# Kernel optimization log

Hardware: AMD Instinct MI355X
Metric: run time of the kernel (lower is better)

Reference implementation:

```python
import jax, jax.numpy as jnp
import numpy as np

M, L = 8, 4            # modules x layers -> N = 32 (module,layer) grids
B, H, W = 16, 128, 128  # batch, grid_height, grid_width
E = 256                # number of axonal connections
N = M * L
SPACINGS = (1, 2)      # multi-scale grid spacings ('local', 'global')
EXC_RATIO, EXC_VAL, INH_VAL = 0.8, 1.0, -0.5
CONN_STRENGTH = 0.1


def setup_inputs() -> dict:
    key = jax.random.key(0)
    k_sp, k_mask, k_w, k_src, k_dst = jax.random.split(key, 5)
    spikes = (jax.random.uniform(k_sp, (N, B, H, W)) < 0.1).astype(jnp.float32)
    # excitatory/inhibitory mask per source node (torch.where(rand < ratio, exc, inh))
    exc_mask = jnp.where(jax.random.uniform(k_mask, (N, H, W)) < EXC_RATIO,
                         jnp.float32(EXC_VAL), jnp.float32(INH_VAL))
    # per-connection learned weight grid: randn(H, W) * strength
    conn_weight = jax.random.normal(k_w, (E, H, W), dtype=jnp.float32) * CONN_STRENGTH
    conn_src = jax.random.randint(k_src, (E,), 0, N, dtype=jnp.int32)
    conn_dst = jax.random.randint(k_dst, (E,), 0, N, dtype=jnp.int32)
    scale_weights = jnp.array([1.0, 0.5], dtype=jnp.float32)
    return {"spikes": spikes, "exc_mask": exc_mask, "conn_weight": conn_weight,
            "scale_weights": scale_weights, "conn_src": conn_src, "conn_dst": conn_dst}


def reference(spikes, exc_mask, conn_weight, scale_weights, conn_src, conn_dst):
    # --- AxonalConnections.forward: modulate, weight, scatter-add per connection ---
    modulated = spikes * exc_mask[:, None, :, :]                 # [N,B,H,W]
    msgs = modulated[conn_src] * conn_weight[:, None, :, :]      # [E,B,H,W]
    axonal = jax.ops.segment_sum(msgs, conn_dst, num_segments=N)  # [N,B,H,W]
    # --- MultiScaleGrid.forward: avg layers per module, shift-add by spacing ---
    avg = spikes.reshape(M, L, B, H, W).mean(axis=1)             # [M,B,H,W]
    grid = jnp.zeros_like(avg)
    for si, p in enumerate(SPACINGS):
        w = scale_weights[si]
        grid = grid.at[p:].add(avg[:-p] * w)   # src i = j - p
        grid = grid.at[:-p].add(avg[p:] * w)   # src i = j + p
    # --- _combine_axonal_and_grid: grid signal broadcast to all layers of module ---
    combined = axonal + jnp.repeat(grid, L, axis=0)              # [N,B,H,W]
    return combined
```

## Files before the change

### kernel.cpp

```cpp
#include <hip/hip_runtime.h>
#include <stdint.h>

#define NMOD 8
#define NLAY 4
#define NN   32
#define NB   16
#define HW   16384
#define BHW  262144
#define NE   256
#define NT   256
#define NGRP 4

__device__ __forceinline__ float lo_bf(uint32_t u) {
    union { uint32_t u32; float f; } v; v.u32 = u << 16; return v.f;
}
__device__ __forceinline__ float hi_bf(uint32_t u) {
    union { uint32_t u32; float f; } v; v.u32 = u & 0xffff0000u; return v.f;
}
__device__ __forceinline__ uint32_t pack_trunc(float a, float b) {
    union { float f; uint32_t u; } x, y; x.f = a; y.f = b;
    return (x.u >> 16) | (y.u & 0xffff0000u);
}
__device__ __forceinline__ uint32_t f2bf(float f) {
    union { float ff; uint32_t u; } v; v.ff = f;
    uint32_t u = v.u;
    u += 0x7fffu + ((u >> 16) & 1u);
    return u >> 16;
}

struct ScsSmem {
    uint32_t mod[NN * NT];
    int off[NN + 1];
    int cnt[NN];
    int pair[NE];
};

extern "C" __global__ void __launch_bounds__(NT) scs_axon_grid_kernel(
    const void* __restrict__ d_spikes,
    const void* __restrict__ d_mask,
    const void* __restrict__ d_connw,
    const void* __restrict__ d_scale,
    const int*  __restrict__ conn_src,
    const int*  __restrict__ conn_dst,
    void*       __restrict__ d_outp)
{
    __shared__ ScsSmem sm;

    const int tid   = threadIdx.x;
    const int idx   = blockIdx.x;
    const int chunk = (idx & 7) + 8 * ((idx >> 9) & 3);
    const int mid   = (idx >> 3) & 63;
    const int b     = mid & 15;
    const int ng    = mid >> 4;
    const int n0    = ng * (NN / NGRP);
    const int hw0   = chunk * (2 * NT) + tid * 2;
    const int hwd   = hw0 >> 1;
    const int spw   = (b * HW + hw0) >> 1;

    const bool is_f32 = (*(const uint32_t*)d_scale) == 0x3F800000u;

    const int my_s = conn_src[tid];
    const int my_d = conn_dst[tid];
    if (tid < NN) sm.cnt[tid] = 0;
    __syncthreads();
    atomicAdd(&sm.cnt[my_d], 1);
    __syncthreads();
    if (tid == 0) {
        int a = 0;
        for (int n = 0; n < NN; ++n) { sm.off[n] = a; a += sm.cnt[n]; }
        sm.off[NN] = a;
    }
    __syncthreads();
    if (tid < NN) sm.cnt[tid] = 0;
    __syncthreads();
    {
        int pos = sm.off[my_d] + atomicAdd(&sm.cnt[my_d], 1);
        sm.pair[pos] = (my_s << 8) | tid;
    }

    float avg0[NMOD], avg1[NMOD];
#pragma unroll
    for (int m = 0; m < NMOD; ++m) { avg0[m] = 0.f; avg1[m] = 0.f; }

    float w1, w2;
    if (is_f32) {
        const float* sc = (const float*)d_scale;
        w1 = sc[0]; w2 = sc[1];
        const float2* sp = (const float2*)d_spikes;
        const float2* mk = (const float2*)d_mask;
#pragma unroll
        for (int n = 0; n < NN; ++n) {
            float2 s = sp[n * (BHW / 2) + spw];
            float2 m = mk[n * (HW / 2) + hwd];
            sm.mod[n * NT + tid] = pack_trunc(s.x * m.x, s.y * m.y);
            avg0[n >> 2] += s.x;
            avg1[n >> 2] += s.y;
        }
    } else {
        const uint16_t* sc = (const uint16_t*)d_scale;
        w1 = lo_bf((uint32_t)sc[0]); w2 = lo_bf((uint32_t)sc[1]);
        const uint32_t* sp = (const uint32_t*)d_spikes;
        const uint32_t* mk = (const uint32_t*)d_mask;
#pragma unroll
        for (int n = 0; n < NN; ++n) {
            uint32_t su = sp[n * (BHW / 2) + spw];
            uint32_t mu = mk[n * (HW / 2) + hwd];
            float s0 = lo_bf(su), s1 = hi_bf(su);
            sm.mod[n * NT + tid] = pack_trunc(s0 * lo_bf(mu), s1 * hi_bf(mu));
            avg0[n >> 2] += s0;
            avg1[n >> 2] += s1;
        }
    }

    float g0[NMOD], g1[NMOD];
#pragma unroll
    for (int m = 0; m < NMOD; ++m) {
        float t0 = 0.f, t1 = 0.f, u0 = 0.f, u1 = 0.f;
        if (m >= 1)        { t0 += avg0[m - 1]; t1 += avg1[m - 1]; }
        if (m + 1 < NMOD)  { t0 += avg0[m + 1]; t1 += avg1[m + 1]; }
        if (m >= 2)        { u0 += avg0[m - 2]; u1 += avg1[m - 2]; }
        if (m + 2 < NMOD)  { u0 += avg0[m + 2]; u1 += avg1[m + 2]; }
        g0[m] = (t0 * w1 + u0 * w2) * 0.25f;
        g1[m] = (t1 * w1 + u1 * w2) * 0.25f;
    }

    __syncthreads();

    if (is_f32) {
        const float2* cw  = (const float2*)d_connw;
        float2*       out = (float2*)d_outp;
#pragma unroll
        for (int i = 0; i < NN / NGRP; ++i) {
            const int n = n0 + i;
            float a0 = g0[n >> 2], a1 = g1[n >> 2];
            const int beg = sm.off[n], end = sm.off[n + 1];
            for (int k = beg; k < end; ++k) {
                const int pk = sm.pair[k];
                float2   wv = cw[(pk & 0xff) * (HW / 2) + hwd];
                uint32_t mv = sm.mod[(pk >> 8) * NT + tid];
                a0 = fmaf(lo_bf(mv), wv.x, a0);
                a1 = fmaf(hi_bf(mv), wv.y, a1);
            }
            float2 o; o.x = a0; o.y = a1;
            out[n * (BHW / 2) + spw] = o;
        }
    } else {
        const uint32_t* cw  = (const uint32_t*)d_connw;
        uint32_t*       out = (uint32_t*)d_outp;
#pragma unroll
        for (int i = 0; i < NN / NGRP; ++i) {
            const int n = n0 + i;
            float a0 = g0[n >> 2], a1 = g1[n >> 2];
            const int beg = __builtin_amdgcn_readfirstlane(sm.off[n]);
            const int end = __builtin_amdgcn_readfirstlane(sm.off[n + 1]);
            int k = beg;
            for (; k + 8 <= end; k += 8) {
                const int p0 = __builtin_amdgcn_readfirstlane(sm.pair[k]);
                const int p1 = __builtin_amdgcn_readfirstlane(sm.pair[k + 1]);
                const int p2 = __builtin_amdgcn_readfirstlane(sm.pair[k + 2]);
                const int p3 = __builtin_amdgcn_readfirstlane(sm.pair[k + 3]);
                const int p4 = __builtin_amdgcn_readfirstlane(sm.pair[k + 4]);
                const int p5 = __builtin_amdgcn_readfirstlane(sm.pair[k + 5]);
                const int p6 = __builtin_amdgcn_readfirstlane(sm.pair[k + 6]);
                const int p7 = __builtin_amdgcn_readfirstlane(sm.pair[k + 7]);
                uint32_t wa = cw[(p0 & 0xff) * (HW / 2) + hwd];
                uint32_t wb = cw[(p1 & 0xff) * (HW / 2) + hwd];
                uint32_t wc = cw[(p2 & 0xff) * (HW / 2) + hwd];
                uint32_t wd = cw[(p3 & 0xff) * (HW / 2) + hwd];
                uint32_t we = cw[(p4 & 0xff) * (HW / 2) + hwd];
                uint32_t wf = cw[(p5 & 0xff) * (HW / 2) + hwd];
                uint32_t wg = cw[(p6 & 0xff) * (HW / 2) + hwd];
                uint32_t wh = cw[(p7 & 0xff) * (HW / 2) + hwd];
                uint32_t ma = sm.mod[(p0 >> 8) * NT + tid];
                uint32_t mb = sm.mod[(p1 >> 8) * NT + tid];
                uint32_t mc = sm.mod[(p2 >> 8) * NT + tid];
                uint32_t md = sm.mod[(p3 >> 8) * NT + tid];
                uint32_t me = sm.mod[(p4 >> 8) * NT + tid];
                uint32_t mf = sm.mod[(p5 >> 8) * NT + tid];
                uint32_t mg = sm.mod[(p6 >> 8) * NT + tid];
                uint32_t mh = sm.mod[(p7 >> 8) * NT + tid];
                a0 = fmaf(lo_bf(ma), lo_bf(wa), a0); a1 = fmaf(hi_bf(ma), hi_bf(wa), a1);
                a0 = fmaf(lo_bf(mb), lo_bf(wb), a0); a1 = fmaf(hi_bf(mb), hi_bf(wb), a1);
                a0 = fmaf(lo_bf(mc), lo_bf(wc), a0); a1 = fmaf(hi_bf(mc), hi_bf(wc), a1);
                a0 = fmaf(lo_bf(md), lo_bf(wd), a0); a1 = fmaf(hi_bf(md), hi_bf(wd), a1);
                a0 = fmaf(lo_bf(me), lo_bf(we), a0); a1 = fmaf(hi_bf(me), hi_bf(we), a1);
                a0 = fmaf(lo_bf(mf), lo_bf(wf), a0); a1 = fmaf(hi_bf(mf), hi_bf(wf), a1);
                a0 = fmaf(lo_bf(mg), lo_bf(wg), a0); a1 = fmaf(hi_bf(mg), hi_bf(wg), a1);
                a0 = fmaf(lo_bf(mh), lo_bf(wh), a0); a1 = fmaf(hi_bf(mh), hi_bf(wh), a1);
            }
            for (; k + 4 <= end; k += 4) {
                const int p0 = __builtin_amdgcn_readfirstlane(sm.pair[k]);
                const int p1 = __builtin_amdgcn_readfirstlane(sm.pair[k + 1]);
                const int p2 = __builtin_amdgcn_readfirstlane(sm.pair[k + 2]);
                const int p3 = __builtin_amdgcn_readfirstlane(sm.pair[k + 3]);
                uint32_t wa = cw[(p0 & 0xff) * (HW / 2) + hwd];
                uint32_t wb = cw[(p1 & 0xff) * (HW / 2) + hwd];
                uint32_t wc = cw[(p2 & 0xff) * (HW / 2) + hwd];
                uint32_t wd = cw[(p3 & 0xff) * (HW / 2) + hwd];
                uint32_t ma = sm.mod[(p0 >> 8) * NT + tid];
                uint32_t mb = sm.mod[(p1 >> 8) * NT + tid];
                uint32_t mc = sm.mod[(p2 >> 8) * NT + tid];
                uint32_t md = sm.mod[(p3 >> 8) * NT + tid];
                a0 = fmaf(lo_bf(ma), lo_bf(wa), a0); a1 = fmaf(hi_bf(ma), hi_bf(wa), a1);
                a0 = fmaf(lo_bf(mb), lo_bf(wb), a0); a1 = fmaf(hi_bf(mb), hi_bf(wb), a1);
                a0 = fmaf(lo_bf(mc), lo_bf(wc), a0); a1 = fmaf(hi_bf(mc), hi_bf(wc), a1);
                a0 = fmaf(lo_bf(md), lo_bf(wd), a0); a1 = fmaf(hi_bf(md), hi_bf(wd), a1);
            }
            for (; k < end; ++k) {
                const int pk = __builtin_amdgcn_readfirstlane(sm.pair[k]);
                uint32_t wv = cw[(pk & 0xff) * (HW / 2) + hwd];
                uint32_t mv = sm.mod[(pk >> 8) * NT + tid];
                a0 = fmaf(lo_bf(mv), lo_bf(wv), a0);
                a1 = fmaf(hi_bf(mv), hi_bf(wv), a1);
            }
            out[n * (BHW / 2) + spw] = f2bf(a0) | (f2bf(a1) << 16);
        }
    }
}

extern "C" void kernel_launch(void* const* d_in, const int* in_sizes, int n_in,
                              void* d_out, int out_size, void* d_ws, size_t ws_size,
                              hipStream_t stream) {
    const int blocks = NB * (HW / (2 * NT)) * NGRP;
    scs_axon_grid_kernel<<<blocks, NT, 0, stream>>>(
        d_in[0], d_in[1], d_in[2], d_in[3],
        (const int*)d_in[4], (const int*)d_in[5], d_out);
}
```

Measured before the change: 145.8 us.

## Stage modulated spikes in two halves to halve shared memory per block

The 32 rows of modulated spikes are now staged in shared memory in two passes of 16 rows, and connections are bucketed by (source half, destination) so each pass only reads rows that are resident. Shared memory per block drops from about 32KB to about 16KB, which is meant to let more blocks run per CU and hide the gather latency. The cost is extra barriers, a second pass over the accumulators, and register-held partial sums. The bf16 path also drops its 8-way unrolled inner loop.

```diff
diff --git a/kernel.cpp b/kernel.cpp
--- a/kernel.cpp
+++ b/kernel.cpp
@@ -10,6 +10,7 @@
 #define NE   256
 #define NT   256
 #define NGRP 4
+#define NROW 16
 
 __device__ __forceinline__ float lo_bf(uint32_t u) {
     union { uint32_t u32; float f; } v; v.u32 = u << 16; return v.f;
@@ -29,9 +30,9 @@
 }
 
 struct ScsSmem {
-    uint32_t mod[NN * NT];
-    int off[NN + 1];
-    int cnt[NN];
+    uint32_t mod[NROW * NT];
+    int off[2 * NN + 1];
+    int cnt[2 * NN];
     int pair[NE];
 };
 
@@ -61,48 +62,115 @@
 
     const int my_s = conn_src[tid];
     const int my_d = conn_dst[tid];
-    if (tid < NN) sm.cnt[tid] = 0;
-    __syncthreads();
-    atomicAdd(&sm.cnt[my_d], 1);
+    const int my_g = ((my_s >> 4) & 1) * NN + my_d;
+    if (tid < 2 * NN) sm.cnt[tid] = 0;
+    __syncthreads();
+    atomicAdd(&sm.cnt[my_g], 1);
     __syncthreads();
     if (tid == 0) {
         int a = 0;
-        for (int n = 0; n < NN; ++n) { sm.off[n] = a; a += sm.cnt[n]; }
-        sm.off[NN] = a;
+        for (int g = 0; g < 2 * NN; ++g) { sm.off[g] = a; a += sm.cnt[g]; }
+        sm.off[2 * NN] = a;
     }
     __syncthreads();
-    if (tid < NN) sm.cnt[tid] = 0;
+    if (tid < 2 * NN) sm.cnt[tid] = 0;
     __syncthreads();
     {
-        int pos = sm.off[my_d] + atomicAdd(&sm.cnt[my_d], 1);
-        sm.pair[pos] = (my_s << 8) | tid;
+        int pos = sm.off[my_g] + atomicAdd(&sm.cnt[my_g], 1);
+        sm.pair[pos] = ((my_s & 15) << 8) | tid;
     }
 
-    float avg0[NMOD], avg1[NMOD];
-#pragma unroll
-    for (int m = 0; m < NMOD; ++m) { avg0[m] = 0.f; avg1[m] = 0.f; }
-
-    float w1, w2;
     if (is_f32) {
         const float* sc = (const float*)d_scale;
-        w1 = sc[0]; w2 = sc[1];
+        const float w1 = sc[0], w2 = sc[1];
         const float2* sp = (const float2*)d_spikes;
         const float2* mk = (const float2*)d_mask;
-#pragma unroll
-        for (int n = 0; n < NN; ++n) {
+        const float2* cw = (const float2*)d_connw;
+        float2*       out = (float2*)d_outp;
+
+        float avg0[NMOD], avg1[NMOD], ac0[NN / NGRP], ac1[NN / NGRP];
+#pragma unroll
+        for (int m = 0; m < NMOD; ++m) { avg0[m] = 0.f; avg1[m] = 0.f; }
+#pragma unroll
+        for (int i = 0; i < NN / NGRP; ++i) { ac0[i] = 0.f; ac1[i] = 0.f; }
+
+#pragma unroll
+        for (int n = 0; n < NROW; ++n) {
             float2 s = sp[n * (BHW / 2) + spw];
             float2 m = mk[n * (HW / 2) + hwd];
             sm.mod[n * NT + tid] = pack_trunc(s.x * m.x, s.y * m.y);
             avg0[n >> 2] += s.x;
             avg1[n >> 2] += s.y;
         }
+        __syncthreads();
+#pragma unroll
+        for (int i = 0; i < NN / NGRP; ++i) {
+            const int n = n0 + i;
+            const int beg = sm.off[n], end = sm.off[n + 1];
+            for (int k = beg; k < end; ++k) {
+                const int pk = sm.pair[k];
+                float2   wv = cw[(pk & 0xff) * (HW / 2) + hwd];
+                uint32_t mv = sm.mod[(pk >> 8) * NT + tid];
+                ac0[i] = fmaf(lo_bf(mv), wv.x, ac0[i]);
+                ac1[i] = fmaf(hi_bf(mv), wv.y, ac1[i]);
+            }
+        }
+        __syncthreads();
+#pragma unroll
+        for (int n = NROW; n < NN; ++n) {
+            float2 s = sp[n * (BHW / 2) + spw];
+            float2 m = mk[n * (HW / 2) + hwd];
+            sm.mod[(n - NROW) * NT + tid] = pack_trunc(s.x * m.x, s.y * m.y);
+            avg0[n >> 2] += s.x;
+            avg1[n >> 2] += s.y;
+        }
+        __syncthreads();
+#pragma unroll
+        for (int i = 0; i < NN / NGRP; ++i) {
+            const int n = n0 + i;
+            const int beg = sm.off[NN + n], end = sm.off[NN + n + 1];
+            for (int k = beg; k < end; ++k) {
+                const int pk = sm.pair[k];
+                float2   wv = cw[(pk & 0xff) * (HW / 2) + hwd];
+                uint32_t mv = sm.mod[(pk >> 8) * NT + tid];
+                ac0[i] = fmaf(lo_bf(mv), wv.x, ac0[i]);
+                ac1[i] = fmaf(hi_bf(mv), wv.y, ac1[i]);
+            }
+        }
+        float g0[NMOD], g1[NMOD];
+#pragma unroll
+        for (int m = 0; m < NMOD; ++m) {
+            float t0 = 0.f, t1 = 0.f, u0 = 0.f, u1 = 0.f;
+            if (m >= 1)        { t0 += avg0[m - 1]; t1 += avg1[m - 1]; }
+            if (m + 1 < NMOD)  { t0 += avg0[m + 1]; t1 += avg1[m + 1]; }
+            if (m >= 2)        { u0 += avg0[m - 2]; u1 += avg1[m - 2]; }
+            if (m + 2 < NMOD)  { u0 += avg0[m + 2]; u1 += avg1[m + 2]; }
+            g0[m] = (t0 * w1 + u0 * w2) * 0.25f;
+            g1[m] = (t1 * w1 + u1 * w2) * 0.25f;
+        }
+#pragma unroll
+        for (int i = 0; i < NN / NGRP; ++i) {
+            const int n = n0 + i;
+            float2 o; o.x = ac0[i] + g0[n >> 2]; o.y = ac1[i] + g1[n >> 2];
+            out[n * (BHW / 2) + spw] = o;
+        }
     } else {
         const uint16_t* sc = (const uint16_t*)d_scale;
-        w1 = lo_bf((uint32_t)sc[0]); w2 = lo_bf((uint32_t)sc[1]);
+        const float w1 = lo_bf((uint32_t)sc[0]);
+        const float w2 = lo_bf((uint32_t)sc[1]);
         const uint32_t* sp = (const uint32_t*)d_spikes;
         const uint32_t* mk = (const uint32_t*)d_mask;
-#pragma unroll
-        for (int n = 0; n < NN; ++n) {
+        const uint32_t* cw = (const uint32_t*)d_connw;
+        uint32_t*       out = (uint32_t*)d_outp;
+
+        float avg0[NMOD], avg1[NMOD], ac0[NN / NGRP], ac1[NN / NGRP];
+#pragma unroll
+        for (int m = 0; m < NMOD; ++m) { avg0[m] = 0.f; avg1[m] = 0.f; }
+#pragma unroll
+        for (int i = 0; i < NN / NGRP; ++i) { ac0[i] = 0.f; ac1[i] = 0.f; }
+
+#pragma unroll
+        for (int n = 0; n < NROW; ++n) {
             uint32_t su = sp[n * (BHW / 2) + spw];
             uint32_t mu = mk[n * (HW / 2) + hwd];
             float s0 = lo_bf(su), s1 = hi_bf(su);
@@ -110,84 +178,14 @@
             avg0[n >> 2] += s0;
             avg1[n >> 2] += s1;
         }
-    }
-
-    float g0[NMOD], g1[NMOD];
-#pragma unroll
-    for (int m = 0; m < NMOD; ++m) {
-        float t0 = 0.f, t1 = 0.f, u0 = 0.f, u1 = 0.f;
-        if (m >= 1)        { t0 += avg0[m - 1]; t1 += avg1[m - 1]; }
-        if (m + 1 < NMOD)  { t0 += avg0[m + 1]; t1 += avg1[m + 1]; }
-        if (m >= 2)        { u0 += avg0[m - 2]; u1 += avg1[m - 2]; }
-        if (m + 2 < NMOD)  { u0 += avg0[m + 2]; u1 += avg1[m + 2]; }
-        g0[m] = (t0 * w1 + u0 * w2) * 0.25f;
-        g1[m] = (t1 * w1 + u1 * w2) * 0.25f;
-    }
-
-    __syncthreads();
-
-    if (is_f32) {
-        const float2* cw  = (const float2*)d_connw;
-        float2*       out = (float2*)d_outp;
-#pragma unroll
-        for (int i = 0; i < NN / NGRP; ++i) {
-            const int n = n0 + i;
-            float a0 = g0[n >> 2], a1 = g1[n >> 2];
-            const int beg = sm.off[n], end = sm.off[n + 1];
-            for (int k = beg; k < end; ++k) {
-                const int pk = sm.pair[k];
-                float2   wv = cw[(pk & 0xff) * (HW / 2) + hwd];
-                uint32_t mv = sm.mod[(pk >> 8) * NT + tid];
-                a0 = fmaf(lo_bf(mv), wv.x, a0);
-                a1 = fmaf(hi_bf(mv), wv.y, a1);
-            }
-            float2 o; o.x = a0; o.y = a1;
-            out[n * (BHW / 2) + spw] = o;
-        }
-    } else {
-        const uint32_t* cw  = (const uint32_t*)d_connw;
-        uint32_t*       out = (uint32_t*)d_outp;
-#pragma unroll
-        for (int i = 0; i < NN / NGRP; ++i) {
-            const int n = n0 + i;
-            float a0 = g0[n >> 2], a1 = g1[n >> 2];
+        __syncthreads();
+#pragma unroll
+        for (int i = 0; i < NN / NGRP; ++i) {
+            const int n = n0 + i;
+            float a0 = ac0[i], a1 = ac1[i];
             const int beg = __builtin_amdgcn_readfirstlane(sm.off[n]);
             const int end = __builtin_amdgcn_readfirstlane(sm.off[n + 1]);
             int k = beg;
-            for (; k + 8 <= end; k += 8) {
-                const int p0 = __builtin_amdgcn_readfirstlane(sm.pair[k]);
-                const int p1 = __builtin_amdgcn_readfirstlane(sm.pair[k + 1]);
-                const int p2 = __builtin_amdgcn_readfirstlane(sm.pair[k + 2]);
-                const int p3 = __builtin_amdgcn_readfirstlane(sm.pair[k + 3]);
-                const int p4 = __builtin_amdgcn_readfirstlane(sm.pair[k + 4]);
-                const int p5 = __builtin_amdgcn_readfirstlane(sm.pair[k + 5]);
-                const int p6 = __builtin_amdgcn_readfirstlane(sm.pair[k + 6]);
-                const int p7 = __builtin_amdgcn_readfirstlane(sm.pair[k + 7]);
-                uint32_t wa = cw[(p0 & 0xff) * (HW / 2) + hwd];
-                uint32_t wb = cw[(p1 & 0xff) * (HW / 2) + hwd];
-                uint32_t wc = cw[(p2 & 0xff) * (HW / 2) + hwd];
-                uint32_t wd = cw[(p3 & 0xff) * (HW / 2) + hwd];
-                uint32_t we = cw[(p4 & 0xff) * (HW / 2) + hwd];
-                uint32_t wf = cw[(p5 & 0xff) * (HW / 2) + hwd];
-                uint32_t wg = cw[(p6 & 0xff) * (HW / 2) + hwd];
-                uint32_t wh = cw[(p7 & 0xff) * (HW / 2) + hwd];
-                uint32_t ma = sm.mod[(p0 >> 8) * NT + tid];
-                uint32_t mb = sm.mod[(p1 >> 8) * NT + tid];
-                uint32_t mc = sm.mod[(p2 >> 8) * NT + tid];
-                uint32_t md = sm.mod[(p3 >> 8) * NT + tid];
-                uint32_t me = sm.mod[(p4 >> 8) * NT + tid];
-                uint32_t mf = sm.mod[(p5 >> 8) * NT + tid];
-                uint32_t mg = sm.mod[(p6 >> 8) * NT + tid];
-                uint32_t mh = sm.mod[(p7 >> 8) * NT + tid];
-                a0 = fmaf(lo_bf(ma), lo_bf(wa), a0); a1 = fmaf(hi_bf(ma), hi_bf(wa), a1);
-                a0 = fmaf(lo_bf(mb), lo_bf(wb), a0); a1 = fmaf(hi_bf(mb), hi_bf(wb), a1);
-                a0 = fmaf(lo_bf(mc), lo_bf(wc), a0); a1 = fmaf(hi_bf(mc), hi_bf(wc), a1);
-                a0 = fmaf(lo_bf(md), lo_bf(wd), a0); a1 = fmaf(hi_bf(md), hi_bf(wd), a1);
-                a0 = fmaf(lo_bf(me), lo_bf(we), a0); a1 = fmaf(hi_bf(me), hi_bf(we), a1);
-                a0 = fmaf(lo_bf(mf), lo_bf(wf), a0); a1 = fmaf(hi_bf(mf), hi_bf(wf), a1);
-                a0 = fmaf(lo_bf(mg), lo_bf(wg), a0); a1 = fmaf(hi_bf(mg), hi_bf(wg), a1);
-                a0 = fmaf(lo_bf(mh), lo_bf(wh), a0); a1 = fmaf(hi_bf(mh), hi_bf(wh), a1);
-            }
             for (; k + 4 <= end; k += 4) {
                 const int p0 = __builtin_amdgcn_readfirstlane(sm.pair[k]);
                 const int p1 = __builtin_amdgcn_readfirstlane(sm.pair[k + 1]);
@@ -213,7 +211,69 @@
                 a0 = fmaf(lo_bf(mv), lo_bf(wv), a0);
                 a1 = fmaf(hi_bf(mv), hi_bf(wv), a1);
             }
-            out[n * (BHW / 2) + spw] = f2bf(a0) | (f2bf(a1) << 16);
+            ac0[i] = a0; ac1[i] = a1;
+        }
+        __syncthreads();
+#pragma unroll
+        for (int n = NROW; n < NN; ++n) {
+            uint32_t su = sp[n * (BHW / 2) + spw];
+            uint32_t mu = mk[n * (HW / 2) + hwd];
+            float s0 = lo_bf(su), s1 = hi_bf(su);
+            sm.mod[(n - NROW) * NT + tid] = pack_trunc(s0 * lo_bf(mu), s1 * hi_bf(mu));
+            avg0[n >> 2] += s0;
+            avg1[n >> 2] += s1;
+        }
+        __syncthreads();
+#pragma unroll
+        for (int i = 0; i < NN / NGRP; ++i) {
+            const int n = n0 + i;
+            float a0 = ac0[i], a1 = ac1[i];
+            const int beg = __builtin_amdgcn_readfirstlane(sm.off[NN + n]);
+            const int end = __builtin_amdgcn_readfirstlane(sm.off[NN + n + 1]);
+            int k = beg;
+            for (; k + 4 <= end; k += 4) {
+                const int p0 = __builtin_amdgcn_readfirstlane(sm.pair[k]);
+                const int p1 = __builtin_amdgcn_readfirstlane(sm.pair[k + 1]);
+                const int p2 = __builtin_amdgcn_readfirstlane(sm.pair[k + 2]);
+                const int p3 = __builtin_amdgcn_readfirstlane(sm.pair[k + 3]);
+                uint32_t wa = cw[(p0 & 0xff) * (HW / 2) + hwd];
+                uint32_t wb = cw[(p1 & 0xff) * (HW / 2) + hwd];
+                uint32_t wc = cw[(p2 & 0xff) * (HW / 2) + hwd];
+                uint32_t wd = cw[(p3 & 0xff) * (HW / 2) + hwd];
+                uint32_t ma = sm.mod[(p0 >> 8) * NT + tid];
+                uint32_t mb = sm.mod[(p1 >> 8) * NT + tid];
+                uint32_t mc = sm.mod[(p2 >> 8) * NT + tid];
+                uint32_t md = sm.mod[(p3 >> 8) * NT + tid];
+                a0 = fmaf(lo_bf(ma), lo_bf(wa), a0); a1 = fmaf(hi_bf(ma), hi_bf(wa), a1);
+                a0 = fmaf(lo_bf(mb), lo_bf(wb), a0); a1 = fmaf(hi_bf(mb), hi_bf(wb), a1);
+                a0 = fmaf(lo_bf(mc), lo_bf(wc), a0); a1 = fmaf(hi_bf(mc), hi_bf(wc), a1);
+                a0 = fmaf(lo_bf(md), lo_bf(wd), a0); a1 = fmaf(hi_bf(md), hi_bf(wd), a1);
+            }
+            for (; k < end; ++k) {
+                const int pk = __builtin_amdgcn_readfirstlane(sm.pair[k]);
+                uint32_t wv = cw[(pk & 0xff) * (HW / 2) + hwd];
+                uint32_t mv = sm.mod[(pk >> 8) * NT + tid];
+                a0 = fmaf(lo_bf(mv), lo_bf(wv), a0);
+                a1 = fmaf(hi_bf(mv), hi_bf(wv), a1);
+            }
+            ac0[i] = a0; ac1[i] = a1;
+        }
+        float g0[NMOD], g1[NMOD];
+#pragma unroll
+        for (int m = 0; m < NMOD; ++m) {
+            float t0 = 0.f, t1 = 0.f, u0 = 0.f, u1 = 0.f;
+            if (m >= 1)        { t0 += avg0[m - 1]; t1 += avg1[m - 1]; }
+            if (m + 1 < NMOD)  { t0 += avg0[m + 1]; t1 += avg1[m + 1]; }
+            if (m >= 2)        { u0 += avg0[m - 2]; u1 += avg1[m - 2]; }
+            if (m + 2 < NMOD)  { u0 += avg0[m + 2]; u1 += avg1[m + 2]; }
+            g0[m] = (t0 * w1 + u0 * w2) * 0.25f;
+            g1[m] = (t1 * w1 + u1 * w2) * 0.25f;
+        }
+#pragma unroll
+        for (int i = 0; i < NN / NGRP; ++i) {
+            const int n = n0 + i;
+            out[n * (BHW / 2) + spw] =
+                f2bf(ac0[i] + g0[n >> 2]) | (f2bf(ac1[i] + g1[n >> 2]) << 16);
         }
     }
 }
```

New measurement: 147.8 us. About the same (+1.4%).
